# Kernel optimization log

Measured on AMD Instinct MI355X. Metric: run time of the kernel, lower is better.

## Reference

```python
import jax, jax.numpy as jnp
import numpy as np
from jax import lax

N_ITER = 50  # SparsemaxBisectFunction hardcodes n_iter=50


def _sparsemax_bisect(X):
    # alpha = 2: gp(x)=x, gp_inv(y)=y, p(x)=clamp(x, 0). X*(alpha-1) == X.
    d = X.shape[-1]
    max_val = jnp.max(X, axis=-1, keepdims=True)
    tau_lo = max_val - 1.0          # max - gp(1)
    tau_hi = max_val - 1.0 / d      # max - gp(1/d)
    f_lo = jnp.sum(jnp.maximum(X - tau_lo, 0.0), axis=-1) - 1.0
    dm = tau_hi - tau_lo

    def body(_, carry):
        tau_lo, dm, _tau_m = carry
        dm = dm * 0.5
        tau_m = tau_lo + dm
        f_m = jnp.sum(jnp.maximum(X - tau_m, 0.0), axis=-1) - 1.0
        mask = (f_m * f_lo >= 0.0)[..., None]
        tau_lo = jnp.where(mask, tau_m, tau_lo)
        return tau_lo, dm, tau_m

    _, _, tau_m = lax.fori_loop(0, N_ITER, body, (tau_lo, dm, tau_lo))
    p = jnp.maximum(X - tau_m, 0.0)  # p_m from the last bisection iteration
    p = p / jnp.sum(p, axis=-1, keepdims=True)  # ensure_sum_one=True
    return p


def setup_inputs() -> dict:
    key = jax.random.key(0)
    X = jax.random.normal(key, (4096, 32000), dtype=jnp.float32)
    return {"X": X}


def reference(X):
    return _sparsemax_bisect(X)
```

## Files before the change

kernel.cpp:

```cpp
#include <hip/hip_runtime.h>
#include <math.h>

constexpr int D = 32000;
constexpr int BLOCK = 1024;
constexpr int NW = BLOCK / 64;
constexpr int FULL4 = D / (4 * BLOCK);
constexpr int REM_ELEMS = D - FULL4 * 4 * BLOCK;
constexpr int REM_THREADS = REM_ELEMS / 4;
constexpr int NV = FULL4 + 1;
constexpr int CAP = 2048;
constexpr int NITER = 50;
constexpr int PERSIST = 256;

__device__ __forceinline__ float wave_sum(float s) {
#pragma unroll
  for (int o = 32; o > 0; o >>= 1) s += __shfl_xor(s, o, 64);
  return s;
}

__device__ __forceinline__ void bar_lds() {
  asm volatile("s_waitcnt lgkmcnt(0)" ::: "memory");
  __builtin_amdgcn_s_barrier();
  asm volatile("" ::: "memory");
}

__device__ __forceinline__ void process_row(
    float4 (&cur)[NV], float4 (&nxt)[NV],
    const float* __restrict__ Xnext, bool pf,
    float* __restrict__ Or,
    float* s_cand, float* s_red, int* s_cnt, int par,
    int t, int lane, int wid, bool has_rem) {
  if (pf) {
    const float4* Xn4 = reinterpret_cast<const float4*>(Xnext);
#pragma unroll
    for (int j = 0; j < FULL4; ++j) nxt[j] = Xn4[t + BLOCK * j];
    if (has_rem)
      nxt[FULL4] = Xn4[FULL4 * BLOCK + t];
    else
      nxt[FULL4] = make_float4(-INFINITY, -INFINITY, -INFINITY, -INFINITY);
  }

  float m = -INFINITY;
#pragma unroll
  for (int j = 0; j < NV; ++j)
    m = fmaxf(m, fmaxf(fmaxf(cur[j].x, cur[j].y), fmaxf(cur[j].z, cur[j].w)));
#pragma unroll
  for (int o = 32; o > 0; o >>= 1) m = fmaxf(m, __shfl_xor(m, o, 64));
  if (lane == 0) s_red[wid] = m;
  bar_lds();
  float rowmax = s_red[0];
#pragma unroll
  for (int j = 1; j < NW; ++j) rowmax = fmaxf(rowmax, s_red[j]);

  const float thresh = rowmax - 1.0f;
#pragma unroll
  for (int j = 0; j < NV; ++j) {
    const float a0 = cur[j].x, a1 = cur[j].y, a2 = cur[j].z, a3 = cur[j].w;
    if (a0 > thresh) { int i = atomicAdd(&s_cnt[par], 1); if (i < CAP) s_cand[i] = a0; }
    if (a1 > thresh) { int i = atomicAdd(&s_cnt[par], 1); if (i < CAP) s_cand[i] = a1; }
    if (a2 > thresh) { int i = atomicAdd(&s_cnt[par], 1); if (i < CAP) s_cand[i] = a2; }
    if (a3 > thresh) { int i = atomicAdd(&s_cnt[par], 1); if (i < CAP) s_cand[i] = a3; }
  }
  bar_lds();
  const int n = s_cnt[par];
  if (t == 0) s_cnt[par ^ 1] = 0;

  float tau, inv;
  if (n <= 64) {
    const float c = (lane < n) ? s_cand[lane] : -INFINITY;
    float tau_lo = rowmax - 1.0f;
    const float tau_hi = rowmax - (1.0f / (float)D);
    float dm = tau_hi - tau_lo;
    const float f_lo = wave_sum(fmaxf(c - tau_lo, 0.0f)) - 1.0f;
    float tau_m = tau_lo;
    for (int it = 0; it < NITER; ++it) {
      dm *= 0.5f;
      tau_m = tau_lo + dm;
      const float f_m = wave_sum(fmaxf(c - tau_m, 0.0f)) - 1.0f;
      if (f_m * f_lo >= 0.0f) tau_lo = tau_m;
    }
    const float sp = wave_sum(fmaxf(c - tau_m, 0.0f));
    tau = tau_m;
    inv = 1.0f / sp;
  } else if (n <= CAP) {
    float tau_lo = rowmax - 1.0f;
    const float tau_hi = rowmax - (1.0f / (float)D);
    float dm = tau_hi - tau_lo;
    float s0 = 0.0f;
    for (int i = lane; i < n; i += 64) s0 += fmaxf(s_cand[i] - tau_lo, 0.0f);
    const float f_lo = wave_sum(s0) - 1.0f;
    float tau_m = tau_lo;
    for (int it = 0; it < NITER; ++it) {
      dm *= 0.5f;
      tau_m = tau_lo + dm;
      float fs = 0.0f;
      for (int i = lane; i < n; i += 64) fs += fmaxf(s_cand[i] - tau_m, 0.0f);
      const float f_m = wave_sum(fs) - 1.0f;
      if (f_m * f_lo >= 0.0f) tau_lo = tau_m;
    }
    float sp = 0.0f;
    for (int i = lane; i < n; i += 64) sp += fmaxf(s_cand[i] - tau_m, 0.0f);
    tau = tau_m;
    inv = 1.0f / wave_sum(sp);
  } else {
    float tau_lo = rowmax - 1.0f;
    const float tau_hi = rowmax - (1.0f / (float)D);
    float dm = tau_hi - tau_lo;
    auto block_fsum = [&](float tt) -> float {
      float s = 0.0f;
#pragma unroll
      for (int j = 0; j < NV; ++j) {
        s += fmaxf(cur[j].x - tt, 0.0f);
        s += fmaxf(cur[j].y - tt, 0.0f);
        s += fmaxf(cur[j].z - tt, 0.0f);
        s += fmaxf(cur[j].w - tt, 0.0f);
      }
      s = wave_sum(s);
      __syncthreads();
      if (lane == 0) s_red[wid] = s;
      __syncthreads();
      float tot = s_red[0];
#pragma unroll
      for (int j = 1; j < NW; ++j) tot += s_red[j];
      return tot;
    };
    const float f_lo = block_fsum(tau_lo) - 1.0f;
    float tau_m = tau_lo;
    for (int it = 0; it < NITER; ++it) {
      dm *= 0.5f;
      tau_m = tau_lo + dm;
      const float f_m = block_fsum(tau_m) - 1.0f;
      if (f_m * f_lo >= 0.0f) tau_lo = tau_m;
    }
    const float sp = block_fsum(tau_m);
    tau = tau_m;
    inv = 1.0f / sp;
  }

#pragma unroll
  for (int j = 0; j < FULL4; ++j) {
    float4 o4;
    o4.x = fmaxf(cur[j].x - tau, 0.0f) * inv;
    o4.y = fmaxf(cur[j].y - tau, 0.0f) * inv;
    o4.z = fmaxf(cur[j].z - tau, 0.0f) * inv;
    o4.w = fmaxf(cur[j].w - tau, 0.0f) * inv;
    *reinterpret_cast<float4*>(Or + 4 * t + 4 * BLOCK * j) = o4;
  }
  if (has_rem) {
    float4 o4;
    o4.x = fmaxf(cur[FULL4].x - tau, 0.0f) * inv;
    o4.y = fmaxf(cur[FULL4].y - tau, 0.0f) * inv;
    o4.z = fmaxf(cur[FULL4].z - tau, 0.0f) * inv;
    o4.w = fmaxf(cur[FULL4].w - tau, 0.0f) * inv;
    *reinterpret_cast<float4*>(Or + 4 * BLOCK * FULL4 + 4 * t) = o4;
  }
}

__global__ __launch_bounds__(BLOCK, 4)
void sparsemax_bisect_kernel(const float* __restrict__ X,
                             float* __restrict__ Out,
                             int rows, int nblk) {
  __shared__ float s_cand[CAP];
  __shared__ float s_red[NW];
  __shared__ int s_cnt[2];

  const int t = threadIdx.x;
  const int lane = t & 63;
  const int wid = t >> 6;
  const bool has_rem = (t < REM_THREADS);

  if (t < 2) s_cnt[t] = 0;

  float4 A[NV], B[NV];

  long r = blockIdx.x;

  {
    const float4* X4 = reinterpret_cast<const float4*>(X + r * (long)D);
#pragma unroll
    for (int j = 0; j < FULL4; ++j) A[j] = X4[t + BLOCK * j];
    A[FULL4] = has_rem
                   ? X4[FULL4 * BLOCK + t]
                   : make_float4(-INFINITY, -INFINITY, -INFINITY, -INFINITY);
  }

  for (;;) {
    long r2 = r + nblk;
    bool pf2 = (r2 < rows);
    process_row(A, B, X + (pf2 ? r2 : r) * (long)D, pf2, Out + r * (long)D,
                s_cand, s_red, s_cnt, 0, t, lane, wid, has_rem);
    if (!pf2) break;
    long r3 = r2 + nblk;
    bool pf3 = (r3 < rows);
    process_row(B, A, X + (pf3 ? r3 : r2) * (long)D, pf3, Out + r2 * (long)D,
                s_cand, s_red, s_cnt, 1, t, lane, wid, has_rem);
    if (!pf3) break;
    r = r3;
  }
}

extern "C" void kernel_launch(void* const* d_in, const int* in_sizes, int n_in,
                              void* d_out, int out_size, void* d_ws, size_t ws_size,
                              hipStream_t stream) {
  const float* X = (const float*)d_in[0];
  float* Out = (float*)d_out;
  const int rows = in_sizes[0] / D;
  const int nblk = rows < PERSIST ? rows : PERSIST;
  hipLaunchKernelGGL(sparsemax_bisect_kernel, dim3(nblk), dim3(BLOCK), 0, stream,
                     X, Out, rows, nblk);
}
```

Baseline: 969.4 us.

## Prefetch next row into LDS via global_load_lds instead of register double-buffer

```diff
diff --git a/kernel.cpp b/kernel.cpp
--- a/kernel.cpp
+++ b/kernel.cpp
@@ -1,14 +1,14 @@
 #include <hip/hip_runtime.h>
 #include <math.h>
+#include <stdint.h>
 
 constexpr int D = 32000;
 constexpr int BLOCK = 1024;
 constexpr int NW = BLOCK / 64;
 constexpr int FULL4 = D / (4 * BLOCK);
-constexpr int REM_ELEMS = D - FULL4 * 4 * BLOCK;
-constexpr int REM_THREADS = REM_ELEMS / 4;
+constexpr int REM_THREADS = (D - FULL4 * 4 * BLOCK) / 4;
 constexpr int NV = FULL4 + 1;
-constexpr int CAP = 2048;
+constexpr int CAP = 1024;
 constexpr int NITER = 50;
 constexpr int PERSIST = 256;
 
@@ -24,142 +24,24 @@
   asm volatile("" ::: "memory");
 }
 
-__device__ __forceinline__ void process_row(
-    float4 (&cur)[NV], float4 (&nxt)[NV],
-    const float* __restrict__ Xnext, bool pf,
-    float* __restrict__ Or,
-    float* s_cand, float* s_red, int* s_cnt, int par,
-    int t, int lane, int wid, bool has_rem) {
-  if (pf) {
-    const float4* Xn4 = reinterpret_cast<const float4*>(Xnext);
-#pragma unroll
-    for (int j = 0; j < FULL4; ++j) nxt[j] = Xn4[t + BLOCK * j];
-    if (has_rem)
-      nxt[FULL4] = Xn4[FULL4 * BLOCK + t];
-    else
-      nxt[FULL4] = make_float4(-INFINITY, -INFINITY, -INFINITY, -INFINITY);
-  }
-
-  float m = -INFINITY;
-#pragma unroll
-  for (int j = 0; j < NV; ++j)
-    m = fmaxf(m, fmaxf(fmaxf(cur[j].x, cur[j].y), fmaxf(cur[j].z, cur[j].w)));
-#pragma unroll
-  for (int o = 32; o > 0; o >>= 1) m = fmaxf(m, __shfl_xor(m, o, 64));
-  if (lane == 0) s_red[wid] = m;
-  bar_lds();
-  float rowmax = s_red[0];
-#pragma unroll
-  for (int j = 1; j < NW; ++j) rowmax = fmaxf(rowmax, s_red[j]);
-
-  const float thresh = rowmax - 1.0f;
-#pragma unroll
-  for (int j = 0; j < NV; ++j) {
-    const float a0 = cur[j].x, a1 = cur[j].y, a2 = cur[j].z, a3 = cur[j].w;
-    if (a0 > thresh) { int i = atomicAdd(&s_cnt[par], 1); if (i < CAP) s_cand[i] = a0; }
-    if (a1 > thresh) { int i = atomicAdd(&s_cnt[par], 1); if (i < CAP) s_cand[i] = a1; }
-    if (a2 > thresh) { int i = atomicAdd(&s_cnt[par], 1); if (i < CAP) s_cand[i] = a2; }
-    if (a3 > thresh) { int i = atomicAdd(&s_cnt[par], 1); if (i < CAP) s_cand[i] = a3; }
-  }
-  bar_lds();
-  const int n = s_cnt[par];
-  if (t == 0) s_cnt[par ^ 1] = 0;
-
-  float tau, inv;
-  if (n <= 64) {
-    const float c = (lane < n) ? s_cand[lane] : -INFINITY;
-    float tau_lo = rowmax - 1.0f;
-    const float tau_hi = rowmax - (1.0f / (float)D);
-    float dm = tau_hi - tau_lo;
-    const float f_lo = wave_sum(fmaxf(c - tau_lo, 0.0f)) - 1.0f;
-    float tau_m = tau_lo;
-    for (int it = 0; it < NITER; ++it) {
-      dm *= 0.5f;
-      tau_m = tau_lo + dm;
-      const float f_m = wave_sum(fmaxf(c - tau_m, 0.0f)) - 1.0f;
-      if (f_m * f_lo >= 0.0f) tau_lo = tau_m;
-    }
-    const float sp = wave_sum(fmaxf(c - tau_m, 0.0f));
-    tau = tau_m;
-    inv = 1.0f / sp;
-  } else if (n <= CAP) {
-    float tau_lo = rowmax - 1.0f;
-    const float tau_hi = rowmax - (1.0f / (float)D);
-    float dm = tau_hi - tau_lo;
-    float s0 = 0.0f;
-    for (int i = lane; i < n; i += 64) s0 += fmaxf(s_cand[i] - tau_lo, 0.0f);
-    const float f_lo = wave_sum(s0) - 1.0f;
-    float tau_m = tau_lo;
-    for (int it = 0; it < NITER; ++it) {
-      dm *= 0.5f;
-      tau_m = tau_lo + dm;
-      float fs = 0.0f;
-      for (int i = lane; i < n; i += 64) fs += fmaxf(s_cand[i] - tau_m, 0.0f);
-      const float f_m = wave_sum(fs) - 1.0f;
-      if (f_m * f_lo >= 0.0f) tau_lo = tau_m;
-    }
-    float sp = 0.0f;
-    for (int i = lane; i < n; i += 64) sp += fmaxf(s_cand[i] - tau_m, 0.0f);
-    tau = tau_m;
-    inv = 1.0f / wave_sum(sp);
-  } else {
-    float tau_lo = rowmax - 1.0f;
-    const float tau_hi = rowmax - (1.0f / (float)D);
-    float dm = tau_hi - tau_lo;
-    auto block_fsum = [&](float tt) -> float {
-      float s = 0.0f;
-#pragma unroll
-      for (int j = 0; j < NV; ++j) {
-        s += fmaxf(cur[j].x - tt, 0.0f);
-        s += fmaxf(cur[j].y - tt, 0.0f);
-        s += fmaxf(cur[j].z - tt, 0.0f);
-        s += fmaxf(cur[j].w - tt, 0.0f);
-      }
-      s = wave_sum(s);
-      __syncthreads();
-      if (lane == 0) s_red[wid] = s;
-      __syncthreads();
-      float tot = s_red[0];
-#pragma unroll
-      for (int j = 1; j < NW; ++j) tot += s_red[j];
-      return tot;
-    };
-    const float f_lo = block_fsum(tau_lo) - 1.0f;
-    float tau_m = tau_lo;
-    for (int it = 0; it < NITER; ++it) {
-      dm *= 0.5f;
-      tau_m = tau_lo + dm;
-      const float f_m = block_fsum(tau_m) - 1.0f;
-      if (f_m * f_lo >= 0.0f) tau_lo = tau_m;
-    }
-    const float sp = block_fsum(tau_m);
-    tau = tau_m;
-    inv = 1.0f / sp;
-  }
-
-#pragma unroll
-  for (int j = 0; j < FULL4; ++j) {
-    float4 o4;
-    o4.x = fmaxf(cur[j].x - tau, 0.0f) * inv;
-    o4.y = fmaxf(cur[j].y - tau, 0.0f) * inv;
-    o4.z = fmaxf(cur[j].z - tau, 0.0f) * inv;
-    o4.w = fmaxf(cur[j].w - tau, 0.0f) * inv;
-    *reinterpret_cast<float4*>(Or + 4 * t + 4 * BLOCK * j) = o4;
-  }
-  if (has_rem) {
-    float4 o4;
-    o4.x = fmaxf(cur[FULL4].x - tau, 0.0f) * inv;
-    o4.y = fmaxf(cur[FULL4].y - tau, 0.0f) * inv;
-    o4.z = fmaxf(cur[FULL4].z - tau, 0.0f) * inv;
-    o4.w = fmaxf(cur[FULL4].w - tau, 0.0f) * inv;
-    *reinterpret_cast<float4*>(Or + 4 * BLOCK * FULL4 + 4 * t) = o4;
-  }
+__device__ __forceinline__ void bar_vm() {
+  asm volatile("s_waitcnt vmcnt(0) lgkmcnt(0)" ::: "memory");
+  __builtin_amdgcn_s_barrier();
+  asm volatile("" ::: "memory");
+}
+
+typedef __attribute__((address_space(3))) void lds_void;
+typedef const __attribute__((address_space(1))) void glb_void;
+
+__device__ __forceinline__ void gload16(const float* g, float* l) {
+  __builtin_amdgcn_global_load_lds((glb_void*)g, (lds_void*)l, 16, 0, 0);
 }
 
 __global__ __launch_bounds__(BLOCK, 4)
 void sparsemax_bisect_kernel(const float* __restrict__ X,
                              float* __restrict__ Out,
                              int rows, int nblk) {
+  __shared__ __attribute__((aligned(16))) float srow[D];
   __shared__ float s_cand[CAP];
   __shared__ float s_red[NW];
   __shared__ int s_cnt[2];
@@ -171,31 +53,165 @@
 
   if (t < 2) s_cnt[t] = 0;
 
-  float4 A[NV], B[NV];
-
   long r = blockIdx.x;
 
   {
-    const float4* X4 = reinterpret_cast<const float4*>(X + r * (long)D);
-#pragma unroll
-    for (int j = 0; j < FULL4; ++j) A[j] = X4[t + BLOCK * j];
-    A[FULL4] = has_rem
-                   ? X4[FULL4 * BLOCK + t]
-                   : make_float4(-INFINITY, -INFINITY, -INFINITY, -INFINITY);
+    const float* Xr = X + r * (long)D;
+#pragma unroll
+    for (int j = 0; j < FULL4; ++j)
+      gload16(Xr + 4 * (j * BLOCK + t), srow + 4 * (j * BLOCK + t));
+    if (has_rem)
+      gload16(Xr + 4 * (FULL4 * BLOCK + t), srow + 4 * (FULL4 * BLOCK + t));
   }
-
+  bar_vm();
+
+  int par = 0;
   for (;;) {
-    long r2 = r + nblk;
-    bool pf2 = (r2 < rows);
-    process_row(A, B, X + (pf2 ? r2 : r) * (long)D, pf2, Out + r * (long)D,
-                s_cand, s_red, s_cnt, 0, t, lane, wid, has_rem);
-    if (!pf2) break;
-    long r3 = r2 + nblk;
-    bool pf3 = (r3 < rows);
-    process_row(B, A, X + (pf3 ? r3 : r2) * (long)D, pf3, Out + r2 * (long)D,
-                s_cand, s_red, s_cnt, 1, t, lane, wid, has_rem);
-    if (!pf3) break;
-    r = r3;
+    const long rn = r + nblk;
+    const bool pf = (rn < rows);
+
+    float4 o[NV];
+#pragma unroll
+    for (int j = 0; j < FULL4; ++j)
+      o[j] = *reinterpret_cast<const float4*>(srow + 4 * (j * BLOCK + t));
+    o[FULL4] =
+        has_rem
+            ? *reinterpret_cast<const float4*>(srow + 4 * (FULL4 * BLOCK + t))
+            : make_float4(-INFINITY, -INFINITY, -INFINITY, -INFINITY);
+#pragma unroll
+    for (int j = 0; j < NV; ++j)
+      asm volatile("" : "+v"(o[j].x), "+v"(o[j].y), "+v"(o[j].z), "+v"(o[j].w));
+    bar_lds();
+
+    if (pf) {
+      const float* Xn = X + rn * (long)D;
+#pragma unroll
+      for (int j = 0; j < FULL4; ++j)
+        gload16(Xn + 4 * (j * BLOCK + t), srow + 4 * (j * BLOCK + t));
+      if (has_rem)
+        gload16(Xn + 4 * (FULL4 * BLOCK + t), srow + 4 * (FULL4 * BLOCK + t));
+    }
+
+    float m = -INFINITY;
+#pragma unroll
+    for (int j = 0; j < NV; ++j)
+      m = fmaxf(m, fmaxf(fmaxf(o[j].x, o[j].y), fmaxf(o[j].z, o[j].w)));
+#pragma unroll
+    for (int off = 32; off > 0; off >>= 1) m = fmaxf(m, __shfl_xor(m, off, 64));
+    if (lane == 0) s_red[wid] = m;
+    bar_lds();
+    float rowmax = s_red[0];
+#pragma unroll
+    for (int j = 1; j < NW; ++j) rowmax = fmaxf(rowmax, s_red[j]);
+
+    const float thresh = rowmax - 1.0f;
+#pragma unroll
+    for (int j = 0; j < NV; ++j) {
+      const float a0 = o[j].x, a1 = o[j].y, a2 = o[j].z, a3 = o[j].w;
+      if (a0 > thresh) { int i = atomicAdd(&s_cnt[par], 1); if (i < CAP) s_cand[i] = a0; }
+      if (a1 > thresh) { int i = atomicAdd(&s_cnt[par], 1); if (i < CAP) s_cand[i] = a1; }
+      if (a2 > thresh) { int i = atomicAdd(&s_cnt[par], 1); if (i < CAP) s_cand[i] = a2; }
+      if (a3 > thresh) { int i = atomicAdd(&s_cnt[par], 1); if (i < CAP) s_cand[i] = a3; }
+    }
+    bar_lds();
+    const int n = s_cnt[par];
+    if (t == 0) s_cnt[par ^ 1] = 0;
+
+    float tau, inv;
+    if (n <= 64) {
+      const float c = (lane < n) ? s_cand[lane] : -INFINITY;
+      float tau_lo = rowmax - 1.0f;
+      const float tau_hi = rowmax - (1.0f / (float)D);
+      float dm = tau_hi - tau_lo;
+      const float f_lo = wave_sum(fmaxf(c - tau_lo, 0.0f)) - 1.0f;
+      float tau_m = tau_lo;
+      for (int it = 0; it < NITER; ++it) {
+        dm *= 0.5f;
+        tau_m = tau_lo + dm;
+        const float f_m = wave_sum(fmaxf(c - tau_m, 0.0f)) - 1.0f;
+        if (f_m * f_lo >= 0.0f) tau_lo = tau_m;
+      }
+      const float sp = wave_sum(fmaxf(c - tau_m, 0.0f));
+      tau = tau_m;
+      inv = 1.0f / sp;
+    } else if (n <= CAP) {
+      float tau_lo = rowmax - 1.0f;
+      const float tau_hi = rowmax - (1.0f / (float)D);
+      float dm = tau_hi - tau_lo;
+      float s0 = 0.0f;
+      for (int i = lane; i < n; i += 64) s0 += fmaxf(s_cand[i] - tau_lo, 0.0f);
+      const float f_lo = wave_sum(s0) - 1.0f;
+      float tau_m = tau_lo;
+      for (int it = 0; it < NITER; ++it) {
+        dm *= 0.5f;
+        tau_m = tau_lo + dm;
+        float fs = 0.0f;
+        for (int i = lane; i < n; i += 64) fs += fmaxf(s_cand[i] - tau_m, 0.0f);
+        const float f_m = wave_sum(fs) - 1.0f;
+        if (f_m * f_lo >= 0.0f) tau_lo = tau_m;
+      }
+      float sp = 0.0f;
+      for (int i = lane; i < n; i += 64) sp += fmaxf(s_cand[i] - tau_m, 0.0f);
+      tau = tau_m;
+      inv = 1.0f / wave_sum(sp);
+    } else {
+      float tau_lo = rowmax - 1.0f;
+      const float tau_hi = rowmax - (1.0f / (float)D);
+      float dm = tau_hi - tau_lo;
+      auto block_fsum = [&](float tt) -> float {
+        float s = 0.0f;
+#pragma unroll
+        for (int j = 0; j < NV; ++j) {
+          s += fmaxf(o[j].x - tt, 0.0f);
+          s += fmaxf(o[j].y - tt, 0.0f);
+          s += fmaxf(o[j].z - tt, 0.0f);
+          s += fmaxf(o[j].w - tt, 0.0f);
+        }
+        s = wave_sum(s);
+        bar_lds();
+        if (lane == 0) s_red[wid] = s;
+        bar_lds();
+        float tot = s_red[0];
+#pragma unroll
+        for (int j = 1; j < NW; ++j) tot += s_red[j];
+        return tot;
+      };
+      const float f_lo = block_fsum(tau_lo) - 1.0f;
+      float tau_m = tau_lo;
+      for (int it = 0; it < NITER; ++it) {
+        dm *= 0.5f;
+        tau_m = tau_lo + dm;
+        const float f_m = block_fsum(tau_m) - 1.0f;
+        if (f_m * f_lo >= 0.0f) tau_lo = tau_m;
+      }
+      const float sp = block_fsum(tau_m);
+      tau = tau_m;
+      inv = 1.0f / sp;
+    }
+
+    float* Or = Out + r * (long)D;
+#pragma unroll
+    for (int j = 0; j < FULL4; ++j) {
+      float4 o4;
+      o4.x = fmaxf(o[j].x - tau, 0.0f) * inv;
+      o4.y = fmaxf(o[j].y - tau, 0.0f) * inv;
+      o4.z = fmaxf(o[j].z - tau, 0.0f) * inv;
+      o4.w = fmaxf(o[j].w - tau, 0.0f) * inv;
+      *reinterpret_cast<float4*>(Or + 4 * (j * BLOCK + t)) = o4;
+    }
+    if (has_rem) {
+      float4 o4;
+      o4.x = fmaxf(o[FULL4].x - tau, 0.0f) * inv;
+      o4.y = fmaxf(o[FULL4].y - tau, 0.0f) * inv;
+      o4.z = fmaxf(o[FULL4].z - tau, 0.0f) * inv;
+      o4.w = fmaxf(o[FULL4].w - tau, 0.0f) * inv;
+      *reinterpret_cast<float4*>(Or + 4 * (FULL4 * BLOCK + t)) = o4;
+    }
+
+    if (!pf) break;
+    r = rn;
+    par ^= 1;
+    bar_vm();
   }
 }
 
```

New measurement: 963.0 us. Within noise of the previous version (-0.7%).
